# Optimization experiments

Hardware: AMD Instinct MI355X
Metric: run time of the kernel (lower is better)

Reference implementation:

```python
import jax, jax.numpy as jnp
import numpy as np

EDGE_TYPES = 5
D = 256      # input_dim == output_dim
HID = 128    # hard-coded hidden size of agg MLPs


def setup_inputs() -> dict:
    key = jax.random.key(0)
    ks = jax.random.split(key, 8)
    B, E, N = 4, 8000, 2000
    edge_distribution = jax.random.uniform(ks[0], (B, E, EDGE_TYPES), dtype=jnp.float32)
    H = jax.random.normal(ks[1], (B, E, N), dtype=jnp.float32)
    ori = jax.random.normal(ks[2], (B, N, D), dtype=jnp.float32)
    # Stacked per-edge-type MLP params: Linear(D->128), ReLU, Linear(128->D)
    W1 = jax.random.normal(ks[3], (EDGE_TYPES, D, HID), dtype=jnp.float32) * (1.0 / np.sqrt(D))
    b1 = jax.random.normal(ks[4], (EDGE_TYPES, HID), dtype=jnp.float32) * 0.01
    W2 = jax.random.normal(ks[5], (EDGE_TYPES, HID, D), dtype=jnp.float32) * (1.0 / np.sqrt(HID))
    b2 = jax.random.normal(ks[6], (EDGE_TYPES, D), dtype=jnp.float32) * 0.01
    return {"edge_distribution": edge_distribution, "H": H, "ori": ori,
            "W1": W1, "b1": b1, "W2": W2, "b2": b2}


def reference(edge_distribution, H, ori, W1, b1, W2, b2):
    # edges = H @ ori : [B, E, D]
    edges = jnp.matmul(H, ori)
    # Per-edge-type 2-layer MLP, vectorized over the type axis t
    h = jax.nn.relu(jnp.einsum('bed,tdh->tbeh', edges, W1) + b1[:, None, None, :])  # [T,B,E,HID]
    mlp_out = jnp.einsum('tbeh,thd->tbed', h, W2) + b2[:, None, None, :]            # [T,B,E,D]
    # Gated accumulate: sum_t edge_distribution[...,t] * mlp_out[t]
    edge_feature = jnp.einsum('bet,tbed->bed', edge_distribution, mlp_out)          # [B,E,D]
    # node_feature = concat(H^T @ edge_feature, ori)
    node_feature = jnp.concatenate(
        [jnp.matmul(jnp.swapaxes(H, 1, 2), edge_feature), ori], axis=-1)            # [B,N,2D]
    return node_feature
```

## Files before the change

### kernel.cpp

```cpp
#include <hip/hip_runtime.h>

typedef unsigned short u16;
typedef short bf16x8 __attribute__((ext_vector_type(8)));
typedef float f32x4 __attribute__((ext_vector_type(4)));
typedef unsigned short u16x8 __attribute__((ext_vector_type(8)));

#define GLL16(gp, lp) __builtin_amdgcn_global_load_lds( \
    (__attribute__((address_space(1))) const unsigned int*)(gp), \
    (__attribute__((address_space(3))) unsigned int*)(lp), 16, 0, 0)

static __device__ __forceinline__ u16 f2bf(float f){
  unsigned u = __builtin_bit_cast(unsigned, f);
  u += 0x7fffu + ((u >> 16) & 1u);
  return (u16)(u >> 16);
}

__global__ void transpose_f32(const float* __restrict__ src, u16* __restrict__ dst,
                              int R, int C, int Rpad, long sB, long dB){
  __shared__ u16 tile[32][33];
  const int b = blockIdx.z;
  src += (long)b*sB; dst += (long)b*dB;
  const int r0 = blockIdx.x*32, c0 = blockIdx.y*32;
  const int j = threadIdx.x & 31, i0 = threadIdx.x >> 5;
  #pragma unroll
  for (int ii=0; ii<32; ii+=8){
    int r = r0+i0+ii, c = c0+j;
    u16 v = 0;
    if (r < R && c < C) v = f2bf(src[(long)r*C + c]);
    tile[i0+ii][j] = v;
  }
  __syncthreads();
  #pragma unroll
  for (int ii=0; ii<32; ii+=8){
    int c = c0+i0+ii, r = r0+j;
    if (c < C && r < Rpad) dst[(long)c*Rpad + r] = tile[j][i0+ii];
  }
}

__global__ void transpose_u16(const u16* __restrict__ src, u16* __restrict__ dst,
                              int R, int C, int Rpad, long sB, long dB){
  __shared__ u16 tile[32][33];
  const int b = blockIdx.z;
  src += (long)b*sB; dst += (long)b*dB;
  const int r0 = blockIdx.x*32, c0 = blockIdx.y*32;
  const int j = threadIdx.x & 31, i0 = threadIdx.x >> 5;
  #pragma unroll
  for (int ii=0; ii<32; ii+=8){
    int r = r0+i0+ii, c = c0+j;
    u16 v = 0;
    if (r < R && c < C) v = src[(long)r*C + c];
    tile[i0+ii][j] = v;
  }
  __syncthreads();
  #pragma unroll
  for (int ii=0; ii<32; ii+=8){
    int c = c0+i0+ii, r = r0+j;
    if (c < C && r < Rpad) dst[(long)c*Rpad + r] = tile[j][i0+ii];
  }
}

__global__ __launch_bounds__(512,2) void g1_kernel(
    const float* __restrict__ Hm, const u16* __restrict__ oriT,
    u16* __restrict__ edges, u16* __restrict__ HT){
  __shared__ u16 As[2][128*32];
  __shared__ u16 Bs[2][256*32];
  __shared__ u16 At[2][32*136];
  const int b = blockIdx.y, bm = blockIdx.x*128;
  const int tid = threadIdx.x;
  const int w = tid>>6, quad = (tid&63)>>4, l16 = tid&15;
  const int wm = (w&1)*64, wn = (w>>1)*64;
  const float* Ab = Hm + (size_t)b*8000*2000 + (size_t)bm*2000;
  const u16*  Bb = oriT + (size_t)b*256*2048;
  u16* HTb = HT + (size_t)b*2048*8000;

  float4 pa[2];
  auto loadA = [&](int kt){
    const int k0 = kt*32;
    #pragma unroll
    for (int i=0;i<2;i++){
      int idx = i*512+tid, row = idx>>3, c4 = (idx&7)*4;
      bool ok = (bm+row < 8000) && (k0+c4 < 2000);
      pa[i] = ok ? *(const float4*)(Ab + (size_t)row*2000 + k0+c4) : make_float4(0.f,0.f,0.f,0.f);
    }
  };
  auto storeA = [&](int kt){
    const int buf = kt&1;
    #pragma unroll
    for (int i=0;i<2;i++){
      int idx = i*512+tid, row = idx>>3, c4 = (idx&7)*4;
      ushort4 o; o.x=f2bf(pa[i].x); o.y=f2bf(pa[i].y); o.z=f2bf(pa[i].z); o.w=f2bf(pa[i].w);
      *(ushort4*)(&As[buf][idx*4]) = o;
      At[buf][(c4+0)*136 + row] = o.x;
      At[buf][(c4+1)*136 + row] = o.y;
      At[buf][(c4+2)*136 + row] = o.z;
      At[buf][(c4+3)*136 + row] = o.w;
    }
  };
  auto stageB = [&](int kt){
    const int buf = kt&1, k0 = kt*32;
    #pragma unroll
    for (int i=0;i<2;i++){
      int idx = i*512+tid;
      int row = idx>>2, c8 = (idx&3)*8;
      GLL16(Bb + (size_t)row*2048 + k0+c8, &Bs[buf][(i*512 + w*64)*8]);
    }
  };

  f32x4 acc[4][4];
  #pragma unroll
  for (int i=0;i<4;i++)
    #pragma unroll
    for (int j=0;j<4;j++) acc[i][j] = (f32x4){0.f,0.f,0.f,0.f};

  loadA(0); stageB(0);
  for (int kt=0; kt<64; kt++){
    storeA(kt);
    __syncthreads();
    if (kt+1 < 64){ loadA(kt+1); stageB(kt+1); }
    const int buf = kt&1, k0 = kt*32;
    {
      int kk = tid>>4, c = tid&15, m0 = c*8;
      if (bm + m0 < 8000){
        u16x8 v = *(const u16x8*)(&At[buf][kk*136 + m0]);
        *(u16x8*)(HTb + (size_t)(k0+kk)*8000 + bm + m0) = v;
      }
    }
    bf16x8 af[4], bf[4];
    #pragma unroll
    for (int mi=0;mi<4;mi++) af[mi] = *(const bf16x8*)(&As[buf][(wm+mi*16+l16)*32 + quad*8]);
    #pragma unroll
    for (int ni=0;ni<4;ni++) bf[ni] = *(const bf16x8*)(&Bs[buf][(wn+ni*16+l16)*32 + quad*8]);
    #pragma unroll
    for (int mi=0;mi<4;mi++)
      #pragma unroll
      for (int ni=0;ni<4;ni++)
        acc[mi][ni] = __builtin_amdgcn_mfma_f32_16x16x32_bf16(af[mi], bf[ni], acc[mi][ni], 0,0,0);
  }
  #pragma unroll
  for (int mi=0;mi<4;mi++){
    #pragma unroll
    for (int r=0;r<4;r++){
      int gm = bm + wm + mi*16 + quad*4 + r;
      if (gm >= 8000) continue;
      u16* dst = edges + ((size_t)b*8000 + gm)*256;
      #pragma unroll
      for (int ni=0;ni<4;ni++) dst[wn + ni*16 + l16] = f2bf(acc[mi][ni][r]);
    }
  }
}

__global__ __launch_bounds__(256,2) void m1_kernel(
    const u16* __restrict__ edges, const u16* __restrict__ W1T,
    const float* __restrict__ b1, const float* __restrict__ edist, u16* __restrict__ H1){
  __shared__ u16 As[2][128*32];
  __shared__ u16 Bs[2][128*32];
  __shared__ float eds[128], b1s[128];
  const int t = blockIdx.y, bm = blockIdx.x*128;
  const int tid = threadIdx.x;
  const int w = tid>>6, quad = (tid&63)>>4, l16 = tid&15;
  const int wm = (w&1)*64, wn = (w>>1)*64;
  if (tid < 128){ eds[tid] = edist[(size_t)(bm+tid)*5 + t]; b1s[tid] = b1[t*128+tid]; }
  const u16* Ab = edges + (size_t)bm*256;
  const u16* Bb = W1T + (size_t)t*128*256;

  auto stage = [&](int kt){
    const int buf = kt&1, k0 = kt*32;
    #pragma unroll
    for (int i=0;i<2;i++){
      int idx = i*256+tid, row = idx>>2, c8 = (idx&3)*8;
      GLL16(Ab + (size_t)row*256 + k0+c8, &As[buf][(i*256 + w*64)*8]);
      GLL16(Bb + (size_t)row*256 + k0+c8, &Bs[buf][(i*256 + w*64)*8]);
    }
  };

  f32x4 acc[4][4];
  #pragma unroll
  for (int i=0;i<4;i++)
    #pragma unroll
    for (int j=0;j<4;j++) acc[i][j] = (f32x4){0.f,0.f,0.f,0.f};

  stage(0);
  for (int kt=0; kt<8; kt++){
    __syncthreads();
    if (kt+1 < 8) stage(kt+1);
    const int buf = kt&1;
    bf16x8 af[4], bf[4];
    #pragma unroll
    for (int mi=0;mi<4;mi++) af[mi] = *(const bf16x8*)(&As[buf][(wm+mi*16+l16)*32 + quad*8]);
    #pragma unroll
    for (int ni=0;ni<4;ni++) bf[ni] = *(const bf16x8*)(&Bs[buf][(wn+ni*16+l16)*32 + quad*8]);
    #pragma unroll
    for (int mi=0;mi<4;mi++)
      #pragma unroll
      for (int ni=0;ni<4;ni++)
        acc[mi][ni] = __builtin_amdgcn_mfma_f32_16x16x32_bf16(af[mi], bf[ni], acc[mi][ni], 0,0,0);
  }
  #pragma unroll
  for (int mi=0;mi<4;mi++){
    #pragma unroll
    for (int r=0;r<4;r++){
      int lrow = wm + mi*16 + quad*4 + r;
      float s = eds[lrow];
      u16* dst = H1 + ((size_t)t*32000 + bm + lrow)*128;
      #pragma unroll
      for (int ni=0;ni<4;ni++){
        int lc = wn + ni*16 + l16;
        float v = fmaxf(acc[mi][ni][r] + b1s[lc], 0.f) * s;
        dst[lc] = f2bf(v);
      }
    }
  }
}

__global__ __launch_bounds__(256,2) void m2_kernel(
    const u16* __restrict__ H1, const u16* __restrict__ W2T,
    const float* __restrict__ b2, const float* __restrict__ edist, u16* __restrict__ EF){
  __shared__ u16 As[2][128*32];
  __shared__ u16 Bs[2][128*32];
  __shared__ float eds[640], b2s[640];
  const int bm = blockIdx.x*128, bn = blockIdx.y*128;
  const int tid = threadIdx.x;
  const int w = tid>>6, quad = (tid&63)>>4, l16 = tid&15;
  const int wm = (w&1)*64, wn = (w>>1)*64;
  for (int i=tid;i<640;i+=256){
    eds[i] = edist[(size_t)bm*5 + i];
    b2s[i] = b2[(i>>7)*256 + bn + (i&127)];
  }
  auto stage = [&](int kt){
    const int buf = kt&1, t = kt>>2, k0 = (kt&3)*32;
    #pragma unroll
    for (int i=0;i<2;i++){
      int idx = i*256+tid, row = idx>>2, c8 = (idx&3)*8;
      GLL16(H1 + ((size_t)t*32000 + bm+row)*128 + k0+c8, &As[buf][(i*256 + w*64)*8]);
      GLL16(W2T + ((size_t)t*256 + bn+row)*128 + k0+c8, &Bs[buf][(i*256 + w*64)*8]);
    }
  };

  f32x4 acc[4][4];
  #pragma unroll
  for (int i=0;i<4;i++)
    #pragma unroll
    for (int j=0;j<4;j++) acc[i][j] = (f32x4){0.f,0.f,0.f,0.f};

  stage(0);
  for (int kt=0; kt<20; kt++){
    __syncthreads();
    if (kt+1 < 20) stage(kt+1);
    const int buf = kt&1;
    bf16x8 af[4], bf[4];
    #pragma unroll
    for (int mi=0;mi<4;mi++) af[mi] = *(const bf16x8*)(&As[buf][(wm+mi*16+l16)*32 + quad*8]);
    #pragma unroll
    for (int ni=0;ni<4;ni++) bf[ni] = *(const bf16x8*)(&Bs[buf][(wn+ni*16+l16)*32 + quad*8]);
    #pragma unroll
    for (int mi=0;mi<4;mi++)
      #pragma unroll
      for (int ni=0;ni<4;ni++)
        acc[mi][ni] = __builtin_amdgcn_mfma_f32_16x16x32_bf16(af[mi], bf[ni], acc[mi][ni], 0,0,0);
  }
  #pragma unroll
  for (int mi=0;mi<4;mi++){
    #pragma unroll
    for (int r=0;r<4;r++){
      int lrow = wm + mi*16 + quad*4 + r;
      float e0=eds[lrow*5+0], e1=eds[lrow*5+1], e2=eds[lrow*5+2], e3=eds[lrow*5+3], e4=eds[lrow*5+4];
      u16* dst = EF + (size_t)(bm+lrow)*256 + bn;
      #pragma unroll
      for (int ni=0;ni<4;ni++){
        int lc = wn + ni*16 + l16;
        float bias = e0*b2s[lc] + e1*b2s[128+lc] + e2*b2s[256+lc] + e3*b2s[384+lc] + e4*b2s[512+lc];
        dst[lc] = f2bf(acc[mi][ni][r] + bias);
      }
    }
  }
}

__global__ __launch_bounds__(512,2) void g3_kernel(
    const u16* __restrict__ HT, const u16* __restrict__ EFt, float* __restrict__ part){
  __shared__ u16 As[2][128*32];
  __shared__ u16 Bs[2][256*32];
  const int bm = blockIdx.x*128, ks = blockIdx.y, b = blockIdx.z;
  const int tid = threadIdx.x;
  const int w = tid>>6, quad = (tid&63)>>4, l16 = tid&15;
  const int wm = (w&1)*64, wn = (w>>1)*64;
  const u16* Ab = HT + (size_t)b*2048*8000 + (size_t)bm*8000;
  const u16* Bb = EFt + (size_t)b*256*8000;
  const int it0 = (250*ks)/4, it1 = (250*(ks+1))/4;

  auto stage = [&](int kt){
    const int buf = kt&1, k0 = kt*32;
    {
      int row = tid>>2, c8 = (tid&3)*8;
      GLL16(Ab + (size_t)row*8000 + k0+c8, &As[buf][(w*64)*8]);
    }
    #pragma unroll
    for (int i=0;i<2;i++){
      int idx = i*512+tid, row = idx>>2, c8 = (idx&3)*8;
      GLL16(Bb + (size_t)row*8000 + k0+c8, &Bs[buf][(i*512 + w*64)*8]);
    }
  };

  f32x4 acc[4][4];
  #pragma unroll
  for (int i=0;i<4;i++)
    #pragma unroll
    for (int j=0;j<4;j++) acc[i][j] = (f32x4){0.f,0.f,0.f,0.f};

  stage(it0);
  for (int kt=it0; kt<it1; kt++){
    __syncthreads();
    if (kt+1 < it1) stage(kt+1);
    const int buf = kt&1;
    bf16x8 af[4], bf[4];
    #pragma unroll
    for (int mi=0;mi<4;mi++) af[mi] = *(const bf16x8*)(&As[buf][(wm+mi*16+l16)*32 + quad*8]);
    #pragma unroll
    for (int ni=0;ni<4;ni++) bf[ni] = *(const bf16x8*)(&Bs[buf][(wn+ni*16+l16)*32 + quad*8]);
    #pragma unroll
    for (int mi=0;mi<4;mi++)
      #pragma unroll
      for (int ni=0;ni<4;ni++)
        acc[mi][ni] = __builtin_amdgcn_mfma_f32_16x16x32_bf16(af[mi], bf[ni], acc[mi][ni], 0,0,0);
  }
  float* dst0 = part + ((size_t)(b*4 + ks)*2048)*256;
  #pragma unroll
  for (int mi=0;mi<4;mi++){
    #pragma unroll
    for (int r=0;r<4;r++){
      int gm = bm + wm + mi*16 + quad*4 + r;
      float* dst = dst0 + (size_t)gm*256;
      #pragma unroll
      for (int ni=0;ni<4;ni++) dst[wn + ni*16 + l16] = acc[mi][ni][r];
    }
  }
}

__global__ void assemble_kernel(const float* __restrict__ part, const float* __restrict__ ori,
                                float* __restrict__ out){
  const int b = blockIdx.y;
  int u = blockIdx.x*256 + threadIdx.x;
  int n = u>>6, c4 = (u&63)*4;
  f32x4 s = (f32x4){0.f,0.f,0.f,0.f};
  #pragma unroll
  for (int ks=0; ks<4; ks++)
    s += *(const f32x4*)(part + ((size_t)(b*4+ks)*2048 + n)*256 + c4);
  float* dst = out + ((size_t)(b*2000+n))*512;
  *(f32x4*)(dst + c4) = s;
  *(f32x4*)(dst + 256 + c4) = *(const f32x4*)(ori + ((size_t)(b*2000+n))*256 + c4);
}

extern "C" void kernel_launch(void* const* d_in, const int* in_sizes, int n_in,
                              void* d_out, int out_size, void* d_ws, size_t ws_size,
                              hipStream_t stream) {
  const float* ed  = (const float*)d_in[0];
  const float* Hm  = (const float*)d_in[1];
  const float* ori = (const float*)d_in[2];
  const float* W1  = (const float*)d_in[3];
  const float* b1  = (const float*)d_in[4];
  const float* W2  = (const float*)d_in[5];
  const float* b2  = (const float*)d_in[6];
  float* out = (float*)d_out;
  char* ws = (char*)d_ws;

  u16* HT    = (u16*)(ws);
  u16* oriT  = (u16*)(ws + 131072000);
  u16* W1T   = (u16*)(ws + 135266304);
  u16* W2T   = (u16*)(ws + 135593984);
  u16* edges = (u16*)(ws + 135921664);
  u16* H1    = (u16*)(ws + 152305664);
  u16* EF    = (u16*)(ws + 193265664);
  u16* EFt   = edges;
  float* part = (float*)H1;

  hipLaunchKernelGGL(transpose_f32, dim3(64,8,4), dim3(256), 0, stream,
                     ori, oriT, 2000, 256, 2048, 512000L, 524288L);
  hipLaunchKernelGGL(transpose_f32, dim3(8,4,5), dim3(256), 0, stream,
                     W1, W1T, 256, 128, 256, 32768L, 32768L);
  hipLaunchKernelGGL(transpose_f32, dim3(4,8,5), dim3(256), 0, stream,
                     W2, W2T, 128, 256, 128, 32768L, 32768L);

  hipLaunchKernelGGL(g1_kernel, dim3(63,4), dim3(512), 0, stream, Hm, oriT, edges, HT);
  hipLaunchKernelGGL(m1_kernel, dim3(250,5), dim3(256), 0, stream, edges, W1T, b1, ed, H1);
  hipLaunchKernelGGL(m2_kernel, dim3(250,2), dim3(256), 0, stream, H1, W2T, b2, ed, EF);
  hipLaunchKernelGGL(transpose_u16, dim3(250,8,4), dim3(256), 0, stream,
                     EF, EFt, 8000, 256, 8000, 2048000L, 2048000L);
  hipLaunchKernelGGL(g3_kernel, dim3(16,4,4), dim3(512), 0, stream, HT, EFt, part);
  hipLaunchKernelGGL(assemble_kernel, dim3(500,4), dim3(256), 0, stream, part, ori, out);

  (void)in_sizes; (void)n_in; (void)ws_size;
}
```

Baseline: 575.4 us.

## Fuse both MLP layers into one kernel with a transposed output, swizzle At, remap g3 grid

```diff
diff --git a/kernel.cpp b/kernel.cpp
--- a/kernel.cpp
+++ b/kernel.cpp
@@ -27,28 +27,6 @@
     int r = r0+i0+ii, c = c0+j;
     u16 v = 0;
     if (r < R && c < C) v = f2bf(src[(long)r*C + c]);
-    tile[i0+ii][j] = v;
-  }
-  __syncthreads();
-  #pragma unroll
-  for (int ii=0; ii<32; ii+=8){
-    int c = c0+i0+ii, r = r0+j;
-    if (c < C && r < Rpad) dst[(long)c*Rpad + r] = tile[j][i0+ii];
-  }
-}
-
-__global__ void transpose_u16(const u16* __restrict__ src, u16* __restrict__ dst,
-                              int R, int C, int Rpad, long sB, long dB){
-  __shared__ u16 tile[32][33];
-  const int b = blockIdx.z;
-  src += (long)b*sB; dst += (long)b*dB;
-  const int r0 = blockIdx.x*32, c0 = blockIdx.y*32;
-  const int j = threadIdx.x & 31, i0 = threadIdx.x >> 5;
-  #pragma unroll
-  for (int ii=0; ii<32; ii+=8){
-    int r = r0+i0+ii, c = c0+j;
-    u16 v = 0;
-    if (r < R && c < C) v = src[(long)r*C + c];
     tile[i0+ii][j] = v;
   }
   __syncthreads();
@@ -90,10 +68,10 @@
       int idx = i*512+tid, row = idx>>3, c4 = (idx&7)*4;
       ushort4 o; o.x=f2bf(pa[i].x); o.y=f2bf(pa[i].y); o.z=f2bf(pa[i].z); o.w=f2bf(pa[i].w);
       *(ushort4*)(&As[buf][idx*4]) = o;
-      At[buf][(c4+0)*136 + row] = o.x;
-      At[buf][(c4+1)*136 + row] = o.y;
-      At[buf][(c4+2)*136 + row] = o.z;
-      At[buf][(c4+3)*136 + row] = o.w;
+      At[buf][(c4+0)*136 + (row ^ ((((c4+0)>>3)&3)<<3))] = o.x;
+      At[buf][(c4+1)*136 + (row ^ ((((c4+1)>>3)&3)<<3))] = o.y;
+      At[buf][(c4+2)*136 + (row ^ ((((c4+2)>>3)&3)<<3))] = o.z;
+      At[buf][(c4+3)*136 + (row ^ ((((c4+3)>>3)&3)<<3))] = o.w;
     }
   };
   auto stageB = [&](int kt){
@@ -121,7 +99,7 @@
     {
       int kk = tid>>4, c = tid&15, m0 = c*8;
       if (bm + m0 < 8000){
-        u16x8 v = *(const u16x8*)(&At[buf][kk*136 + m0]);
+        u16x8 v = *(const u16x8*)(&At[buf][kk*136 + (m0 ^ (((kk>>3)&3)<<3))]);
         *(u16x8*)(HTb + (size_t)(k0+kk)*8000 + bm + m0) = v;
       }
     }
@@ -149,127 +127,115 @@
   }
 }
 
-__global__ __launch_bounds__(256,2) void m1_kernel(
-    const u16* __restrict__ edges, const u16* __restrict__ W1T,
-    const float* __restrict__ b1, const float* __restrict__ edist, u16* __restrict__ H1){
-  __shared__ u16 As[2][128*32];
-  __shared__ u16 Bs[2][128*32];
-  __shared__ float eds[128], b1s[128];
-  const int t = blockIdx.y, bm = blockIdx.x*128;
+__global__ __launch_bounds__(512,2) void mlp_kernel(
+    const u16* __restrict__ edges, const u16* __restrict__ W1T, const u16* __restrict__ W2T,
+    const float* __restrict__ b1, const float* __restrict__ b2,
+    const float* __restrict__ edist, u16* __restrict__ EFt){
+  __shared__ u16 Es[8*4096];
+  __shared__ u16 Hs[4*4096];
+  __shared__ u16 Bs[2][256*32];
+  __shared__ float eds[640], b1s[640], b2s[1280];
+  const int bm = blockIdx.x*128;
   const int tid = threadIdx.x;
   const int w = tid>>6, quad = (tid&63)>>4, l16 = tid&15;
-  const int wm = (w&1)*64, wn = (w>>1)*64;
-  if (tid < 128){ eds[tid] = edist[(size_t)(bm+tid)*5 + t]; b1s[tid] = b1[t*128+tid]; }
-  const u16* Ab = edges + (size_t)bm*256;
-  const u16* Bb = W1T + (size_t)t*128*256;
-
-  auto stage = [&](int kt){
-    const int buf = kt&1, k0 = kt*32;
-    #pragma unroll
-    for (int i=0;i<2;i++){
-      int idx = i*256+tid, row = idx>>2, c8 = (idx&3)*8;
-      GLL16(Ab + (size_t)row*256 + k0+c8, &As[buf][(i*256 + w*64)*8]);
-      GLL16(Bb + (size_t)row*256 + k0+c8, &Bs[buf][(i*256 + w*64)*8]);
-    }
-  };
-
-  f32x4 acc[4][4];
+  const int wm1 = (w&1)*64, wh1 = (w>>1)*32;
+  const int wd2 = (w&3)*64, wm2 = (w>>2)*64;
+
+  for (int i=tid;i<640;i+=512){ eds[i] = edist[(size_t)bm*5 + i]; b1s[i] = b1[i]; }
+  for (int i=tid;i<1280;i+=512) b2s[i] = b2[i];
+
+  const u16* Eb = edges + (size_t)bm*256;
+  {
+    int row = tid>>2, c8 = (tid&3)*8;
+    #pragma unroll
+    for (int kt=0;kt<8;kt++)
+      GLL16(Eb + (size_t)row*256 + kt*32 + c8, &Es[kt*4096 + (w*64)*8]);
+  }
+
+  auto stage1 = [&](int t, int kt){
+    const int buf = kt&1;
+    int row = tid>>2, c8 = (tid&3)*8;
+    GLL16(W1T + ((size_t)t*128 + row)*256 + kt*32 + c8, &Bs[buf][(w*64)*8]);
+  };
+  auto stage2 = [&](int t, int kk){
+    const int buf = kk&1;
+    #pragma unroll
+    for (int i=0;i<2;i++){
+      int idx = i*512+tid, row = idx>>2, c8 = (idx&3)*8;
+      GLL16(W2T + ((size_t)t*256 + row)*128 + kk*32 + c8, &Bs[buf][(i*512 + w*64)*8]);
+    }
+  };
+
+  f32x4 acc2[4][4];
   #pragma unroll
   for (int i=0;i<4;i++)
     #pragma unroll
-    for (int j=0;j<4;j++) acc[i][j] = (f32x4){0.f,0.f,0.f,0.f};
-
-  stage(0);
-  for (int kt=0; kt<8; kt++){
+    for (int j=0;j<4;j++) acc2[i][j] = (f32x4){0.f,0.f,0.f,0.f};
+
+  stage1(0,0);
+  for (int t=0;t<5;t++){
+    f32x4 acc1[4][2];
+    #pragma unroll
+    for (int i=0;i<4;i++){ acc1[i][0] = (f32x4){0.f,0.f,0.f,0.f}; acc1[i][1] = (f32x4){0.f,0.f,0.f,0.f}; }
+    for (int kt=0;kt<8;kt++){
+      __syncthreads();
+      if (kt<7) stage1(t,kt+1); else stage2(t,0);
+      const int buf = kt&1;
+      bf16x8 af[4], bfr[2];
+      #pragma unroll
+      for (int mi=0;mi<4;mi++) af[mi] = *(const bf16x8*)(&Es[kt*4096 + (wm1+mi*16+l16)*32 + quad*8]);
+      #pragma unroll
+      for (int ni=0;ni<2;ni++) bfr[ni] = *(const bf16x8*)(&Bs[buf][(wh1+ni*16+l16)*32 + quad*8]);
+      #pragma unroll
+      for (int mi=0;mi<4;mi++)
+        #pragma unroll
+        for (int ni=0;ni<2;ni++)
+          acc1[mi][ni] = __builtin_amdgcn_mfma_f32_16x16x32_bf16(af[mi], bfr[ni], acc1[mi][ni], 0,0,0);
+    }
     __syncthreads();
-    if (kt+1 < 8) stage(kt+1);
-    const int buf = kt&1;
-    bf16x8 af[4], bf[4];
-    #pragma unroll
-    for (int mi=0;mi<4;mi++) af[mi] = *(const bf16x8*)(&As[buf][(wm+mi*16+l16)*32 + quad*8]);
-    #pragma unroll
-    for (int ni=0;ni<4;ni++) bf[ni] = *(const bf16x8*)(&Bs[buf][(wn+ni*16+l16)*32 + quad*8]);
-    #pragma unroll
-    for (int mi=0;mi<4;mi++)
-      #pragma unroll
-      for (int ni=0;ni<4;ni++)
-        acc[mi][ni] = __builtin_amdgcn_mfma_f32_16x16x32_bf16(af[mi], bf[ni], acc[mi][ni], 0,0,0);
+    #pragma unroll
+    for (int mi=0;mi<4;mi++){
+      #pragma unroll
+      for (int r=0;r<4;r++){
+        int lrow = wm1 + mi*16 + quad*4 + r;
+        float s = eds[lrow*5 + t];
+        #pragma unroll
+        for (int ni=0;ni<2;ni++){
+          int ch = wh1 + ni*16 + l16;
+          float v = fmaxf(acc1[mi][ni][r] + b1s[t*128 + ch], 0.f) * s;
+          Hs[(w>>1)*4096 + lrow*32 + (ni*16 + l16)] = f2bf(v);
+        }
+      }
+    }
+    for (int kk=0;kk<4;kk++){
+      __syncthreads();
+      if (kk<3) stage2(t,kk+1); else if (t<4) stage1(t+1,0);
+      const int buf = kk&1;
+      bf16x8 af2[4], bf2[4];
+      #pragma unroll
+      for (int mi=0;mi<4;mi++) af2[mi] = *(const bf16x8*)(&Bs[buf][(wd2+mi*16+l16)*32 + quad*8]);
+      #pragma unroll
+      for (int ni=0;ni<4;ni++) bf2[ni] = *(const bf16x8*)(&Hs[kk*4096 + (wm2+ni*16+l16)*32 + quad*8]);
+      #pragma unroll
+      for (int mi=0;mi<4;mi++)
+        #pragma unroll
+        for (int ni=0;ni<4;ni++)
+          acc2[mi][ni] = __builtin_amdgcn_mfma_f32_16x16x32_bf16(af2[mi], bf2[ni], acc2[mi][ni], 0,0,0);
+    }
   }
   #pragma unroll
   for (int mi=0;mi<4;mi++){
     #pragma unroll
     for (int r=0;r<4;r++){
-      int lrow = wm + mi*16 + quad*4 + r;
-      float s = eds[lrow];
-      u16* dst = H1 + ((size_t)t*32000 + bm + lrow)*128;
+      int d = wd2 + mi*16 + quad*4 + r;
       #pragma unroll
       for (int ni=0;ni<4;ni++){
-        int lc = wn + ni*16 + l16;
-        float v = fmaxf(acc[mi][ni][r] + b1s[lc], 0.f) * s;
-        dst[lc] = f2bf(v);
-      }
-    }
-  }
-}
-
-__global__ __launch_bounds__(256,2) void m2_kernel(
-    const u16* __restrict__ H1, const u16* __restrict__ W2T,
-    const float* __restrict__ b2, const float* __restrict__ edist, u16* __restrict__ EF){
-  __shared__ u16 As[2][128*32];
-  __shared__ u16 Bs[2][128*32];
-  __shared__ float eds[640], b2s[640];
-  const int bm = blockIdx.x*128, bn = blockIdx.y*128;
-  const int tid = threadIdx.x;
-  const int w = tid>>6, quad = (tid&63)>>4, l16 = tid&15;
-  const int wm = (w&1)*64, wn = (w>>1)*64;
-  for (int i=tid;i<640;i+=256){
-    eds[i] = edist[(size_t)bm*5 + i];
-    b2s[i] = b2[(i>>7)*256 + bn + (i&127)];
-  }
-  auto stage = [&](int kt){
-    const int buf = kt&1, t = kt>>2, k0 = (kt&3)*32;
-    #pragma unroll
-    for (int i=0;i<2;i++){
-      int idx = i*256+tid, row = idx>>2, c8 = (idx&3)*8;
-      GLL16(H1 + ((size_t)t*32000 + bm+row)*128 + k0+c8, &As[buf][(i*256 + w*64)*8]);
-      GLL16(W2T + ((size_t)t*256 + bn+row)*128 + k0+c8, &Bs[buf][(i*256 + w*64)*8]);
-    }
-  };
-
-  f32x4 acc[4][4];
-  #pragma unroll
-  for (int i=0;i<4;i++)
-    #pragma unroll
-    for (int j=0;j<4;j++) acc[i][j] = (f32x4){0.f,0.f,0.f,0.f};
-
-  stage(0);
-  for (int kt=0; kt<20; kt++){
-    __syncthreads();
-    if (kt+1 < 20) stage(kt+1);
-    const int buf = kt&1;
-    bf16x8 af[4], bf[4];
-    #pragma unroll
-    for (int mi=0;mi<4;mi++) af[mi] = *(const bf16x8*)(&As[buf][(wm+mi*16+l16)*32 + quad*8]);
-    #pragma unroll
-    for (int ni=0;ni<4;ni++) bf[ni] = *(const bf16x8*)(&Bs[buf][(wn+ni*16+l16)*32 + quad*8]);
-    #pragma unroll
-    for (int mi=0;mi<4;mi++)
-      #pragma unroll
-      for (int ni=0;ni<4;ni++)
-        acc[mi][ni] = __builtin_amdgcn_mfma_f32_16x16x32_bf16(af[mi], bf[ni], acc[mi][ni], 0,0,0);
-  }
-  #pragma unroll
-  for (int mi=0;mi<4;mi++){
-    #pragma unroll
-    for (int r=0;r<4;r++){
-      int lrow = wm + mi*16 + quad*4 + r;
-      float e0=eds[lrow*5+0], e1=eds[lrow*5+1], e2=eds[lrow*5+2], e3=eds[lrow*5+3], e4=eds[lrow*5+4];
-      u16* dst = EF + (size_t)(bm+lrow)*256 + bn;
-      #pragma unroll
-      for (int ni=0;ni<4;ni++){
-        int lc = wn + ni*16 + l16;
-        float bias = e0*b2s[lc] + e1*b2s[128+lc] + e2*b2s[256+lc] + e3*b2s[384+lc] + e4*b2s[512+lc];
-        dst[lc] = f2bf(acc[mi][ni][r] + bias);
+        int mc = wm2 + ni*16 + l16;
+        float bias = eds[mc*5+0]*b2s[d] + eds[mc*5+1]*b2s[256+d] + eds[mc*5+2]*b2s[512+d]
+                   + eds[mc*5+3]*b2s[768+d] + eds[mc*5+4]*b2s[1024+d];
+        int e = bm + mc;
+        int bq = e / 8000;
+        EFt[((size_t)bq*256 + d)*8000 + (e - bq*8000)] = f2bf(acc2[mi][ni][r] + bias);
       }
     }
   }
@@ -279,7 +245,8 @@
     const u16* __restrict__ HT, const u16* __restrict__ EFt, float* __restrict__ part){
   __shared__ u16 As[2][128*32];
   __shared__ u16 Bs[2][256*32];
-  const int bm = blockIdx.x*128, ks = blockIdx.y, b = blockIdx.z;
+  const int wg = ((int)blockIdx.x & 7)*32 + ((int)blockIdx.x >> 3);
+  const int bm = (wg & 15)*128, ks = (wg>>4)&3, b = wg>>6;
   const int tid = threadIdx.x;
   const int w = tid>>6, quad = (tid&63)>>4, l16 = tid&15;
   const int wm = (w&1)*64, wn = (w>>1)*64;
@@ -367,10 +334,8 @@
   u16* W1T   = (u16*)(ws + 135266304);
   u16* W2T   = (u16*)(ws + 135593984);
   u16* edges = (u16*)(ws + 135921664);
-  u16* H1    = (u16*)(ws + 152305664);
-  u16* EF    = (u16*)(ws + 193265664);
-  u16* EFt   = edges;
-  float* part = (float*)H1;
+  u16* EFt   = (u16*)(ws + 152305664);
+  float* part = (float*)(ws + 168689664);
 
   hipLaunchKernelGGL(transpose_f32, dim3(64,8,4), dim3(256), 0, stream,
                      ori, oriT, 2000, 256, 2048, 512000L, 524288L);
@@ -380,11 +345,9 @@
                      W2, W2T, 128, 256, 128, 32768L, 32768L);
 
   hipLaunchKernelGGL(g1_kernel, dim3(63,4), dim3(512), 0, stream, Hm, oriT, edges, HT);
-  hipLaunchKernelGGL(m1_kernel, dim3(250,5), dim3(256), 0, stream, edges, W1T, b1, ed, H1);
-  hipLaunchKernelGGL(m2_kernel, dim3(250,2), dim3(256), 0, stream, H1, W2T, b2, ed, EF);
-  hipLaunchKernelGGL(transpose_u16, dim3(250,8,4), dim3(256), 0, stream,
-                     EF, EFt, 8000, 256, 8000, 2048000L, 2048000L);
-  hipLaunchKernelGGL(g3_kernel, dim3(16,4,4), dim3(512), 0, stream, HT, EFt, part);
+  hipLaunchKernelGGL(mlp_kernel, dim3(250), dim3(512), 0, stream,
+                     edges, W1T, W2T, b1, b2, ed, EFt);
+  hipLaunchKernelGGL(g3_kernel, dim3(256), dim3(512), 0, stream, HT, EFt, part);
   hipLaunchKernelGGL(assemble_kernel, dim3(500,4), dim3(256), 0, stream, part, ori, out);
 
   (void)in_sizes; (void)n_in; (void)ws_size;
```

Result: faster. 543.6 us (-5.5%).
